# Kernel optimization log

Measured on AMD Instinct MI355X. Metric: run time of the kernel, lower is better.

## Reference

```python
import jax, jax.numpy as jnp
import numpy as np
from jax import lax

# ---- quantum-kernel constants: flipped model f = Tr[rho(theta) O(patch)] ----
# rho(theta) = (I + sum_i theta_i P_i)/4 over the 15 non-identity 2-qubit Paulis.
# O(patch)  = (M + M^T)/2 where M is the 3x3 patch zero-padded to 16 and reshaped 4x4.
# Both are linear in their inputs, so precompute A[i,k] = Re Tr[P_i O(e_k)] and
# t0[k] = Tr[O(e_k)] once on the host.

def _pauli_features():
    I = np.eye(2, dtype=np.complex64)
    X = np.array([[0, 1], [1, 0]], np.complex64)
    Y = np.array([[0, -1j], [1j, 0]], np.complex64)
    Z = np.array([[1, 0], [0, -1]], np.complex64)
    singles = [I, X, Y, Z]
    paulis = [np.kron(a, b) for a in singles for b in singles][1:]  # 15 non-identity
    A = np.zeros((15, 9), np.float32)
    t0 = np.zeros((9,), np.float32)
    for k in range(9):
        M = np.zeros((4, 4), np.complex64)
        M.flat[k] = 1.0
        O = (M + M.conj().T) / 2.0
        t0[k] = float(np.real(np.trace(O)))
        for i, P in enumerate(paulis):
            A[i, k] = float(np.real(np.trace(P @ O)))
    return A, t0

_A_NP, _T0_NP = _pauli_features()
STRIDE = 1
PAD = (1, 1)  # (pad_h, pad_w)


def setup_inputs() -> dict:
    key = jax.random.key(0)
    k1, k2, k3 = jax.random.split(key, 3)
    x = jax.random.normal(k1, (32, 16, 128, 128), dtype=jnp.float32)
    weight = jax.random.normal(k2, (64, 16, 15), dtype=jnp.float32)
    bias = jax.random.normal(k3, (64, 1), dtype=jnp.float32)
    return {"x": x, "weight": weight, "bias": bias}


def reference(x, weight, bias):
    B, C, H, W = x.shape
    ph, pw = PAD
    Ho = (H - 3 + 2 * ph) // STRIDE + 1
    Wo = (W - 3 + 2 * pw) // STRIDE + 1
    # im2col: [B, C*9, Ho, Wo], channel-major (C slowest, 3x3 row-major fastest)
    patches = lax.conv_general_dilated_patches(
        x, (3, 3), (STRIDE, STRIDE), ((ph, ph), (pw, pw)))
    patches = patches.reshape(B, C, 9, Ho * Wo)  # [B, C, 9, P]

    A = jnp.asarray(_A_NP)    # [15, 9]
    t0 = jnp.asarray(_T0_NP)  # [9]

    # identity part of rho: sum over in-channels of Tr[O]/4 (weight-independent)
    base = jnp.einsum('k,bckp->bp', t0, patches)            # [B, P]
    # Pauli features Tr[P_i O(patch)] per (channel, patch)
    qf = jnp.einsum('ik,bckp->bcip', A, patches)            # [B, C, 15, P]
    out = (base[:, None, :] + jnp.einsum('oci,bcip->bop', weight, qf)) * 0.25
    out = out + bias                                        # bias [O,1] -> [B,O,P]
    return out.reshape(B, weight.shape[0], Ho, Wo)
```

## Files before the change

### kernel.cpp

```cpp
#include <hip/hip_runtime.h>
#include <hip/hip_bf16.h>


typedef short bf16x8 __attribute__((ext_vector_type(8)));
typedef float f32x4 __attribute__((ext_vector_type(4)));

__device__ __forceinline__ void pauli_entry(int s, int r, int c, float& re, float& im) {
    re = 0.f; im = 0.f;
    if (s == 0)      { if (r == c) re = 1.f; }
    else if (s == 1) { if (r != c) re = 1.f; }
    else if (s == 2) { if (r == 0 && c == 1) im = -1.f; else if (r == 1 && c == 0) im = 1.f; }
    else             { if (r == c) re = (r == 0) ? 1.f : -1.f; }
}

__device__ __forceinline__ float A_entry(int i, int k) {
    int j = i + 1, sa = j >> 2, sb = j & 3;
    int r = k >> 2, c = k & 3;
    float ar, ai, br, bi;
    pauli_entry(sa, r >> 1, c >> 1, ar, ai);
    pauli_entry(sb, r & 1, c & 1, br, bi);
    float re1 = ar * br - ai * bi;
    pauli_entry(sa, c >> 1, r >> 1, ar, ai);
    pauli_entry(sb, c & 1, r & 1, br, bi);
    float re2 = ar * br - ai * bi;
    return 0.5f * (re1 + re2);
}

__device__ __forceinline__ short f2bf(float f) {
    union { float f; unsigned int u; } a; a.f = f;
    unsigned int r = a.u + 0x7fffu + ((a.u >> 16) & 1u);
    return (short)(r >> 16);
}

__global__ __launch_bounds__(256) void prep_kernel(const float* __restrict__ weight,
                                                   short* __restrict__ afrag) {
    int t = blockIdx.x * 256 + threadIdx.x;
    if (t >= 1280) return;
    int lane = t & 63;
    int mt   = (t >> 6) & 3;
    int ch   = t >> 8;
    int quad = lane >> 4;
    int m    = mt * 16 + (lane & 15);
    short vals[8];
    #pragma unroll
    for (int j = 0; j < 8; ++j) {
        int k = ch * 32 + quad * 8 + j;
        float v = 0.f;
        if (k < 144) {
            int c  = k / 9;
            int k9 = k - 9 * c;
            float acc = (k9 == 0 || k9 == 5) ? 1.f : 0.f;
            const float* w = weight + (m * 16 + c) * 15;
            #pragma unroll
            for (int i = 0; i < 15; ++i) acc += w[i] * A_entry(i, k9);
            v = 0.25f * acc;
        }
        vals[j] = f2bf(v);
    }
    *(bf16x8*)(afrag + t * 8) = *(bf16x8*)vals;
}

__global__ __launch_bounds__(256) void conv_mfma(const float* __restrict__ x,
                                                 const short* __restrict__ afrag,
                                                 const float* __restrict__ bias,
                                                 float* __restrict__ out) {
    __shared__ float sx[48 * 136];
    __shared__ short sa[1280 * 8];

    const int tid = threadIdx.x;
    const int h   = blockIdx.x;
    const int b   = blockIdx.y;

    #pragma unroll
    for (int j = 0; j < 5; ++j) {
        int vid = tid + j * 256;
        *(bf16x8*)(sa + vid * 8) = *(const bf16x8*)(afrag + vid * 8);
    }
    const float* xb = x + (size_t)b * 16 * 128 * 128;
    #pragma unroll
    for (int j = 0; j < 6; ++j) {
        int vid = tid + j * 256;
        int row = vid >> 5;
        int v   = vid & 31;
        int c   = row / 3;
        int kh  = row - 3 * c;
        int hp  = h - 1 + kh;
        float4 val = make_float4(0.f, 0.f, 0.f, 0.f);
        if (hp >= 0 && hp < 128)
            val = *(const float4*)(xb + (c * 128 + hp) * 128 + v * 4);
        *(float4*)(sx + row * 136 + 4 + v * 4) = val;
    }
    if (tid < 48) {
        *(float4*)(sx + tid * 136)       = make_float4(0.f, 0.f, 0.f, 0.f);
        *(float4*)(sx + tid * 136 + 132) = make_float4(0.f, 0.f, 0.f, 0.f);
    }
    __syncthreads();

    const int lane  = tid & 63;
    const int wave  = tid >> 6;
    const int quad  = lane >> 4;
    const int nlo   = lane & 15;
    const int wbase = wave * 32 + nlo;

    f32x4 acc[2][4] = {};

    #pragma unroll
    for (int ch = 0; ch < 5; ++ch) {
        float b0[8], b1[8];
        #pragma unroll
        for (int j = 0; j < 8; ++j) {
            int k  = ch * 32 + quad * 8 + j;
            int kc = (k < 144) ? k : 0;
            int c  = kc / 9;
            int r9 = kc - 9 * c;
            int kh = r9 / 3;
            int kw = r9 - 3 * kh;
            const float* p = sx + (c * 3 + kh) * 136 + 3 + kw + wbase;
            b0[j] = p[0];
            b1[j] = p[16];
        }
        bf16x8 bf0, bf1;
        #pragma unroll
        for (int j = 0; j < 8; ++j) { bf0[j] = f2bf(b0[j]); bf1[j] = f2bf(b1[j]); }
        #pragma unroll
        for (int mt = 0; mt < 4; ++mt) {
            bf16x8 af = *(const bf16x8*)(sa + ((ch * 4 + mt) * 64 + lane) * 8);
            acc[0][mt] = __builtin_amdgcn_mfma_f32_16x16x32_bf16(af, bf0, acc[0][mt], 0, 0, 0);
            acc[1][mt] = __builtin_amdgcn_mfma_f32_16x16x32_bf16(af, bf1, acc[1][mt], 0, 0, 0);
        }
    }

    #pragma unroll
    for (int mt = 0; mt < 4; ++mt) {
        f32x4 bv = *(const f32x4*)(bias + mt * 16 + quad * 4);
        float* dst = out + (((size_t)b * 64 + mt * 16 + quad * 4) * 128 + h) * 128;
        #pragma unroll
        for (int reg = 0; reg < 4; ++reg) {
            float* d = dst + (size_t)reg * 128 * 128;
            d[wbase]      = acc[0][mt][reg] + bv[reg];
            d[wbase + 16] = acc[1][mt][reg] + bv[reg];
        }
    }
}

extern "C" void kernel_launch(void* const* d_in, const int* in_sizes, int n_in,
                              void* d_out, int out_size, void* d_ws, size_t ws_size,
                              hipStream_t stream) {
    const float* x      = (const float*)d_in[0];
    const float* weight = (const float*)d_in[1];
    const float* bias   = (const float*)d_in[2];
    float* out   = (float*)d_out;
    short* afrag = (short*)d_ws;

    prep_kernel<<<5, 256, 0, stream>>>(weight, afrag);
    dim3 grid(128, 32);
    conv_mfma<<<grid, 256, 0, stream>>>(x, afrag, bias, out);
}
```

Baseline: 196.1 us.

## Process four output rows per block with register-resident A fragments

Each block now computes four output rows (one per wave) instead of one, staging six input rows per channel in shared memory so the halo rows are reused across the rows. The A fragments are held in registers per lane instead of being copied to shared memory, and the im2col offsets are precomputed and packed. The bias is folded into the accumulator init, and conversion uses a packed bf16 intrinsic where available. This cuts redundant x loads and LDS traffic at the cost of higher register pressure and a smaller grid of 1024 blocks.

```diff
diff --git a/kernel.cpp b/kernel.cpp
--- a/kernel.cpp
+++ b/kernel.cpp
@@ -32,6 +32,20 @@
     return (short)(r >> 16);
 }
 
+__device__ __forceinline__ unsigned pk_bf16(float a, float b) {
+#if __has_builtin(__builtin_amdgcn_cvt_pk_bf16_f32)
+    typedef __bf16 bf2 __attribute__((ext_vector_type(2)));
+    bf2 r = __builtin_amdgcn_cvt_pk_bf16_f32(a, b);
+    union { bf2 v; unsigned u; } cv; cv.v = r;
+    return cv.u;
+#else
+    union { float f; unsigned u; } x, y; x.f = a; y.f = b;
+    unsigned ra = x.u + 0x7fffu + ((x.u >> 16) & 1u);
+    unsigned rb = y.u + 0x7fffu + ((y.u >> 16) & 1u);
+    return (ra >> 16) | (rb & 0xffff0000u);
+#endif
+}
+
 __global__ __launch_bounds__(256) void prep_kernel(const float* __restrict__ weight,
                                                    short* __restrict__ afrag) {
     int t = blockIdx.x * 256 + threadIdx.x;
@@ -64,81 +78,105 @@
                                                  const short* __restrict__ afrag,
                                                  const float* __restrict__ bias,
                                                  float* __restrict__ out) {
-    __shared__ float sx[48 * 136];
-    __shared__ short sa[1280 * 8];
+    __shared__ float sx[16 * 6 * 136];
 
-    const int tid = threadIdx.x;
-    const int h   = blockIdx.x;
-    const int b   = blockIdx.y;
+    const int tid  = threadIdx.x;
+    const int h0   = blockIdx.x * 4;
+    const int b    = blockIdx.y;
+    const int lane = tid & 63;
+    const int wave = tid >> 6;
+    const int quad = lane >> 4;
+    const int nlo  = lane & 15;
 
+    bf16x8 Areg[20];
     #pragma unroll
-    for (int j = 0; j < 5; ++j) {
-        int vid = tid + j * 256;
-        *(bf16x8*)(sa + vid * 8) = *(const bf16x8*)(afrag + vid * 8);
-    }
+    for (int i = 0; i < 20; ++i)
+        Areg[i] = *(const bf16x8*)(afrag + (i * 64 + lane) * 8);
+
     const float* xb = x + (size_t)b * 16 * 128 * 128;
     #pragma unroll
-    for (int j = 0; j < 6; ++j) {
+    for (int j = 0; j < 12; ++j) {
         int vid = tid + j * 256;
         int row = vid >> 5;
         int v   = vid & 31;
-        int c   = row / 3;
-        int kh  = row - 3 * c;
-        int hp  = h - 1 + kh;
+        int c   = row / 6;
+        int r   = row - 6 * c;
+        int hp  = h0 - 1 + r;
         float4 val = make_float4(0.f, 0.f, 0.f, 0.f);
         if (hp >= 0 && hp < 128)
             val = *(const float4*)(xb + (c * 128 + hp) * 128 + v * 4);
         *(float4*)(sx + row * 136 + 4 + v * 4) = val;
     }
-    if (tid < 48) {
-        *(float4*)(sx + tid * 136)       = make_float4(0.f, 0.f, 0.f, 0.f);
-        *(float4*)(sx + tid * 136 + 132) = make_float4(0.f, 0.f, 0.f, 0.f);
+    if (tid < 192) {
+        int row = tid >> 1, side = tid & 1;
+        *(float4*)(sx + row * 136 + (side ? 132 : 0)) = make_float4(0.f, 0.f, 0.f, 0.f);
+    }
+
+    unsigned offp[20];
+    #pragma unroll
+    for (int ch = 0; ch < 5; ++ch) {
+        #pragma unroll
+        for (int j2 = 0; j2 < 4; ++j2) {
+            unsigned o01[2];
+            #pragma unroll
+            for (int t = 0; t < 2; ++t) {
+                int k = ch * 32 + quad * 8 + j2 * 2 + t;
+                if (k >= 144) k = 0;
+                int c  = k / 9, r9 = k - 9 * c;
+                int kh = r9 / 3, kw = r9 - 3 * kh;
+                o01[t] = (unsigned)((c * 6 + wave + kh) * 136 + 3 + kw + nlo);
+            }
+            offp[ch * 4 + j2] = o01[0] | (o01[1] << 16);
+        }
     }
     __syncthreads();
 
-    const int lane  = tid & 63;
-    const int wave  = tid >> 6;
-    const int quad  = lane >> 4;
-    const int nlo   = lane & 15;
-    const int wbase = wave * 32 + nlo;
+    const int h = h0 + wave;
+    #pragma unroll
+    for (int np = 0; np < 4; ++np) {
+        const int pixadd = np * 32;
 
-    f32x4 acc[2][4] = {};
-
-    #pragma unroll
-    for (int ch = 0; ch < 5; ++ch) {
-        float b0[8], b1[8];
-        #pragma unroll
-        for (int j = 0; j < 8; ++j) {
-            int k  = ch * 32 + quad * 8 + j;
-            int kc = (k < 144) ? k : 0;
-            int c  = kc / 9;
-            int r9 = kc - 9 * c;
-            int kh = r9 / 3;
-            int kw = r9 - 3 * kh;
-            const float* p = sx + (c * 3 + kh) * 136 + 3 + kw + wbase;
-            b0[j] = p[0];
-            b1[j] = p[16];
-        }
-        bf16x8 bf0, bf1;
-        #pragma unroll
-        for (int j = 0; j < 8; ++j) { bf0[j] = f2bf(b0[j]); bf1[j] = f2bf(b1[j]); }
+        f32x4 acc[2][4];
         #pragma unroll
         for (int mt = 0; mt < 4; ++mt) {
-            bf16x8 af = *(const bf16x8*)(sa + ((ch * 4 + mt) * 64 + lane) * 8);
-            acc[0][mt] = __builtin_amdgcn_mfma_f32_16x16x32_bf16(af, bf0, acc[0][mt], 0, 0, 0);
-            acc[1][mt] = __builtin_amdgcn_mfma_f32_16x16x32_bf16(af, bf1, acc[1][mt], 0, 0, 0);
+            f32x4 bv = *(const f32x4*)(bias + mt * 16 + quad * 4);
+            acc[0][mt] = bv;
+            acc[1][mt] = bv;
         }
-    }
 
-    #pragma unroll
-    for (int mt = 0; mt < 4; ++mt) {
-        f32x4 bv = *(const f32x4*)(bias + mt * 16 + quad * 4);
-        float* dst = out + (((size_t)b * 64 + mt * 16 + quad * 4) * 128 + h) * 128;
         #pragma unroll
-        for (int reg = 0; reg < 4; ++reg) {
-            float* d = dst + (size_t)reg * 128 * 128;
-            d[wbase]      = acc[0][mt][reg] + bv[reg];
-            d[wbase + 16] = acc[1][mt][reg] + bv[reg];
+        for (int ch = 0; ch < 5; ++ch) {
+            unsigned b0p[4], b1p[4];
+            #pragma unroll
+            for (int j2 = 0; j2 < 4; ++j2) {
+                unsigned pk = offp[ch * 4 + j2];
+                const float* p0 = sx + (pk & 0xffffu) + pixadd;
+                const float* p1 = sx + (pk >> 16) + pixadd;
+                float a0 = p0[0], a1 = p0[16];
+                float c0 = p1[0], c1 = p1[16];
+                b0p[j2] = pk_bf16(a0, c0);
+                b1p[j2] = pk_bf16(a1, c1);
+            }
+            union { unsigned u[4]; bf16x8 v; } B0, B1;
+            #pragma unroll
+            for (int j2 = 0; j2 < 4; ++j2) { B0.u[j2] = b0p[j2]; B1.u[j2] = b1p[j2]; }
+            #pragma unroll
+            for (int mt = 0; mt < 4; ++mt) {
+                acc[0][mt] = __builtin_amdgcn_mfma_f32_16x16x32_bf16(Areg[ch * 4 + mt], B0.v, acc[0][mt], 0, 0, 0);
+                acc[1][mt] = __builtin_amdgcn_mfma_f32_16x16x32_bf16(Areg[ch * 4 + mt], B1.v, acc[1][mt], 0, 0, 0);
+            }
+        }
+
+        const int wp = pixadd + nlo;
+        #pragma unroll
+        for (int mt = 0; mt < 4; ++mt) {
+            float* dst = out + (((size_t)b * 64 + mt * 16 + quad * 4) * 128 + h) * 128;
+            #pragma unroll
+            for (int reg = 0; reg < 4; ++reg) {
+                float* d = dst + (size_t)reg * 128 * 128;
+                d[wp]      = acc[0][mt][reg];
+                d[wp + 16] = acc[1][mt][reg];
+            }
         }
     }
 }
@@ -153,6 +191,6 @@
     short* afrag = (short*)d_ws;
 
     prep_kernel<<<5, 256, 0, stream>>>(weight, afrag);
-    dim3 grid(128, 32);
+    dim3 grid(32, 32);
     conv_mfma<<<grid, 256, 0, stream>>>(x, afrag, bias, out);
 }
```

Measured after the change: 174.6 us. 11.0% less time.
